# Optimization experiments

Hardware: AMD Instinct MI355X
Metric: run time of the kernel (lower is better)

## Reference

```python
import jax, jax.numpy as jnp
import numpy as np

B, C_IN, C_OUT, H, W = 4, 256, 256, 56, 56
NH, K, P = 2, 5, 2
HD = C_OUT // NH          # 128
SE_H = C_OUT // 16        # 16
SE_H2 = max(SE_H // 16, 1)  # 1
EPS = 1e-5


def setup_inputs() -> dict:
    key = jax.random.key(0)
    ks = jax.random.split(key, 16)
    n = lambda k, sh, s=1.0: jax.random.normal(k, sh, jnp.float32) * s

    def bn_params(k, c):
        k1, k2 = jax.random.split(k)
        return (1.0 + 0.1 * n(k1, (c,)), 0.1 * n(k2, (c,)),
                jnp.zeros((c,), jnp.float32), jnp.ones((c,), jnp.float32))

    agg_g1, agg_b1, agg_m1, agg_v1 = bn_params(ks[6], C_OUT)
    agg_g2, agg_b2, agg_m2, agg_v2 = bn_params(ks[7], C_OUT)
    se_g_in, se_b_in, se_m_in, se_v_in = bn_params(ks[8], SE_H)
    se_g_out, se_b_out, se_m_out, se_v_out = bn_params(ks[9], C_OUT)
    return {
        "x": n(ks[0], (B, C_IN, H, W)),
        "Wq": n(ks[1], (C_OUT, C_IN), C_IN ** -0.5),
        "Wk": n(ks[2], (C_OUT, C_IN), C_IN ** -0.5),
        "Wv": n(ks[3], (C_OUT, C_IN), C_IN ** -0.5),
        "rel_h": n(ks[4], (HD, 1, 1, K, 1)),
        "rel_w": n(ks[5], (HD, 1, 1, 1, K)),
        "agg_g1": agg_g1, "agg_b1": agg_b1, "agg_m1": agg_m1, "agg_v1": agg_v1,
        "agg_W": n(ks[10], (C_OUT, C_OUT), C_OUT ** -0.5),
        "agg_g2": agg_g2, "agg_b2": agg_b2, "agg_m2": agg_m2, "agg_v2": agg_v2,
        "se_Win": n(ks[11], (SE_H, C_OUT), C_OUT ** -0.5),
        "se_g_in": se_g_in, "se_b_in": se_b_in, "se_m_in": se_m_in, "se_v_in": se_v_in,
        "se_fc1": n(ks[12], (SE_H2, SE_H), SE_H ** -0.5),
        "se_fc2": n(ks[13], (SE_H, SE_H2)),
        "se_Wout": n(ks[14], (C_OUT, SE_H), SE_H ** -0.5),
        "se_g_out": se_g_out, "se_b_out": se_b_out, "se_m_out": se_m_out, "se_v_out": se_v_out,
    }


def _conv1x1(Wm, t):
    return jnp.einsum('oc,bchw->bohw', Wm, t)


def _bn(t, g, b, m, v):
    # eval-mode BatchNorm2d with running stats
    return (t - m[:, None, None]) * (g * jax.lax.rsqrt(v + EPS))[:, None, None] + b[:, None, None]


def _windows(t):
    # (B, O, H+2P, W+2P) -> (B, O, H, W, K, K), matching torch unfold(2,K,1).unfold(3,K,1)
    w = jnp.stack([t[:, :, i:i + H, j:j + W] for i in range(K) for j in range(K)], axis=-1)
    return w.reshape(t.shape[0], t.shape[1], H, W, K, K)


def reference(x, Wq, Wk, Wv, rel_h, rel_w,
              agg_g1, agg_b1, agg_m1, agg_v1, agg_W, agg_g2, agg_b2, agg_m2, agg_v2,
              se_Win, se_g_in, se_b_in, se_m_in, se_v_in, se_fc1, se_fc2, se_Wout,
              se_g_out, se_b_out, se_m_out, se_v_out):
    xp = jnp.pad(x, ((0, 0), (0, 0), (P, P), (P, P)))
    q = _conv1x1(Wq, x).reshape(B, NH, HD, H, W)          # (B,NH,HD,H,W)
    k_win = _windows(_conv1x1(Wk, xp))                    # (B,O,H,W,K,K)
    v_win = _windows(_conv1x1(Wv, xp))
    # relative position bias: first head gets rel_h (height taps), second gets rel_w
    k_win = jnp.concatenate([k_win[:, :HD] + rel_h[None], k_win[:, HD:] + rel_w[None]], axis=1)
    k_r = k_win.reshape(B, NH, HD, H, W, K * K)
    v_r = v_win.reshape(B, NH, HD, H, W, K * K)
    scores = jnp.einsum('bnchw,bnchwk->bnhwk', q, k_r) / jnp.sqrt(jnp.float32(HD))
    attn = jax.nn.softmax(scores, axis=-1)
    out = jnp.einsum('bnhwk,bnchwk->bnchw', attn, v_r).reshape(B, C_OUT, H, W)
    # agg: BN -> ReLU -> 1x1 conv -> BN
    y = jax.nn.relu(_bn(out, agg_g1, agg_b1, agg_m1, agg_v1))
    y = _bn(_conv1x1(agg_W, y), agg_g2, agg_b2, agg_m2, agg_v2)
    # squeeze-excitation (intended math; original view(b,c) is a channel-count bug)
    s = jax.nn.relu(_bn(_conv1x1(se_Win, y), se_g_in, se_b_in, se_m_in, se_v_in))  # (B,SE_H,H,W)
    p = s.mean(axis=(2, 3))                                                        # (B,SE_H)
    g = jax.nn.sigmoid(jax.nn.relu(p @ se_fc1.T) @ se_fc2.T)                       # (B,SE_H)
    s = s * g[:, :, None, None]
    return _bn(_conv1x1(se_Wout, s), se_g_out, se_b_out, se_m_out, se_v_out)
```

## Files before the change

### kernel.cpp

```cpp
#include <hip/hip_runtime.h>
#include <hip/hip_bf16.h>

#define HW 3136
#define HH 56
#define WW 56
#define BB 4
#define CC 256
#define HD 128

#define TH 4
#define TW 8
#define WR 8
#define WC 12
#define WPX 96
#define KS2 136

#define ASTR 72

typedef __attribute__((ext_vector_type(8))) short bf16x8;
typedef __attribute__((ext_vector_type(4))) float f32x4;

__device__ __forceinline__ unsigned short f2bf(float f) {
    unsigned int u; __builtin_memcpy(&u, &f, 4);
    unsigned int r = u + 0x7FFFu + ((u >> 16) & 1u);
    return (unsigned short)(r >> 16);
}
__device__ __forceinline__ float bflo(unsigned int u) {
    unsigned int x = u << 16; float f; __builtin_memcpy(&f, &x, 4); return f;
}
__device__ __forceinline__ float bfhi(unsigned int u) {
    unsigned int x = u & 0xFFFF0000u; float f; __builtin_memcpy(&f, &x, 4); return f;
}
__device__ __forceinline__ void unpk8(uint4 u, float* f) {
    f[0] = bflo(u.x); f[1] = bfhi(u.x); f[2] = bflo(u.y); f[3] = bfhi(u.y);
    f[4] = bflo(u.z); f[5] = bfhi(u.z); f[6] = bflo(u.w); f[7] = bfhi(u.w);
}

__global__ __launch_bounds__(256) void cvt_all(
    const float* __restrict__ x,
    const float* __restrict__ Wq, const float* __restrict__ Wk,
    const float* __restrict__ Wv, const float* __restrict__ Wa,
    const float* __restrict__ Wse,
    const float* __restrict__ rel_h, const float* __restrict__ rel_w,
    unsigned short* __restrict__ xt, unsigned short* __restrict__ wb,
    float* __restrict__ psum, float* __restrict__ relws)
{
    int t = threadIdx.x;
    if (blockIdx.z == 4) {
        int bid = blockIdx.y * 49 + blockIdx.x;
        if (bid == 0 && t < 64) psum[t] = 0.f;
        if (bid == 1 && t < 128) {
#pragma unroll
            for (int tt = 0; tt < 5; tt++) {
                relws[tt * 128 + t]       = rel_h[t * 5 + tt];
                relws[640 + tt * 128 + t] = rel_w[t * 5 + tt];
            }
        }
        for (int chunk = bid; chunk < 260; chunk += 196) {
            int wsel, off;
            if (chunk < 256) { wsel = chunk >> 6; off = (chunk & 63) * 1024 + t * 4; }
            else             { wsel = 4;          off = (chunk - 256) * 1024 + t * 4; }
            const float* s = (wsel == 0) ? Wq : (wsel == 1) ? Wk :
                             (wsel == 2) ? Wv : (wsel == 3) ? Wa : Wse;
            float4 f = *(const float4*)(s + off);
            uint2 pk;
            pk.x = (unsigned int)f2bf(f.x) | ((unsigned int)f2bf(f.y) << 16);
            pk.y = (unsigned int)f2bf(f.z) | ((unsigned int)f2bf(f.w) << 16);
            *(uint2*)(wb + (size_t)wsel * 65536 + off) = pk;
        }
        return;
    }
    int b = blockIdx.z;
    int c0 = blockIdx.y * 64;
    int p0 = blockIdx.x * 64;
    __shared__ float tile[64][65];
    int p4 = t & 15, cl = t >> 4;
    const float* xb = x + ((size_t)b * CC + c0) * HW + p0;
#pragma unroll
    for (int i = 0; i < 4; i++) {
        int c = cl + 16 * i;
        float4 f = *(const float4*)(xb + (size_t)c * HW + p4 * 4);
        tile[c][p4 * 4 + 0] = f.x; tile[c][p4 * 4 + 1] = f.y;
        tile[c][p4 * 4 + 2] = f.z; tile[c][p4 * 4 + 3] = f.w;
    }
    __syncthreads();
    int c2 = t & 31, pl = t >> 5;
    unsigned short* xo = xt + ((size_t)b * HW + p0) * CC + c0;
#pragma unroll
    for (int i = 0; i < 8; i++) {
        int p = pl + 8 * i;
        float a = tile[2 * c2][p], bb = tile[2 * c2 + 1][p];
        unsigned int pk = (unsigned int)f2bf(a) | ((unsigned int)f2bf(bb) << 16);
        *(unsigned int*)(xo + (size_t)p * CC + 2 * c2) = pk;
    }
}

__global__ __launch_bounds__(256) void qkv_mfma(
    const unsigned short* __restrict__ xt, const unsigned short* __restrict__ wqkv,
    unsigned short* __restrict__ q_ws, unsigned short* __restrict__ k_ws,
    unsigned short* __restrict__ v_ws)
{
    int wsel = blockIdx.z;
    unsigned short* outp = (wsel == 0) ? q_ws : ((wsel == 1) ? k_ws : v_ws);
    int gp0 = blockIdx.x * 128, o0 = blockIdx.y * 128;

    __shared__ unsigned short As[128 * ASTR];
    __shared__ unsigned short Bs[128 * ASTR];
    const unsigned short* xb = xt + (size_t)gp0 * CC;
    const unsigned short* wbp = wqkv + (size_t)wsel * 65536 + (size_t)o0 * CC;

    int t = threadIdx.x;
    int wave = t >> 6, lane = t & 63;
    int mo = (wave & 1) * 64, no = (wave >> 1) * 64;
    int lm = lane & 15, lq = lane >> 4;
    int sr = t >> 3, sc = t & 7;

    f32x4 acc[4][4];
#pragma unroll
    for (int i = 0; i < 4; i++)
#pragma unroll
        for (int j = 0; j < 4; j++) acc[i][j] = (f32x4){0.f, 0.f, 0.f, 0.f};

    for (int k0 = 0; k0 < 256; k0 += 64) {
#pragma unroll
        for (int i = 0; i < 4; i++) {
            int r = sr + 32 * i;
            *(uint4*)&As[r * ASTR + sc * 8] = *(const uint4*)(xb + (size_t)r * CC + k0 + sc * 8);
            *(uint4*)&Bs[r * ASTR + sc * 8] = *(const uint4*)(wbp + (size_t)r * CC + k0 + sc * 8);
        }
        __syncthreads();
#pragma unroll
        for (int ks = 0; ks < 64; ks += 32) {
            bf16x8 af[4], bfr[4];
#pragma unroll
            for (int i = 0; i < 4; i++)
                af[i] = *(bf16x8*)&As[(mo + 16 * i + lm) * ASTR + ks + lq * 8];
#pragma unroll
            for (int j = 0; j < 4; j++)
                bfr[j] = *(bf16x8*)&Bs[(no + 16 * j + lm) * ASTR + ks + lq * 8];
#pragma unroll
            for (int i = 0; i < 4; i++)
#pragma unroll
                for (int j = 0; j < 4; j++)
                    acc[i][j] = __builtin_amdgcn_mfma_f32_16x16x32_bf16(
                        af[i], bfr[j], acc[i][j], 0, 0, 0);
        }
        __syncthreads();
    }
    unsigned short* ob = outp + (size_t)gp0 * CC + o0;
    bool ev = (lm & 1) == 0;
    int elm = lm & ~1;
#pragma unroll
    for (int i = 0; i < 4; i++)
#pragma unroll
        for (int j = 0; j < 4; j++)
#pragma unroll
            for (int r = 0; r < 4; r++) {
                float v = acc[i][j][r];
                float p = __shfl_xor(v, 1, 64);
                unsigned int pk = ev
                    ? ((unsigned int)f2bf(v) | ((unsigned int)f2bf(p) << 16))
                    : ((unsigned int)f2bf(p) | ((unsigned int)f2bf(v) << 16));
                if (ev == (r < 2)) {
                    int m = mo + 16 * i + lq * 4 + r;
                    int n = no + 16 * j + elm;
                    *(unsigned int*)(ob + (size_t)m * CC + n) = pk;
                }
            }
}

__global__ __launch_bounds__(256) void agg_mfma(
    const unsigned short* __restrict__ ao, const unsigned short* __restrict__ wagg,
    const float* __restrict__ g1, const float* __restrict__ b1,
    const float* __restrict__ m1, const float* __restrict__ v1,
    const float* __restrict__ g2, const float* __restrict__ b2,
    const float* __restrict__ m2, const float* __restrict__ v2,
    float* __restrict__ y2)
{
    int gp0 = blockIdx.x * 128, o0 = blockIdx.y * 128;

    __shared__ unsigned short As[128 * ASTR];
    __shared__ unsigned short Bs[128 * ASTR];
    __shared__ float s1[256], o1[256], s2[256], o2[256];

    int t = threadIdx.x;
    {
        float sc1 = g1[t] * rsqrtf(v1[t] + 1e-5f);
        s1[t] = sc1; o1[t] = b1[t] - m1[t] * sc1;
        float sc2 = g2[t] * rsqrtf(v2[t] + 1e-5f);
        s2[t] = sc2; o2[t] = b2[t] - m2[t] * sc2;
    }

    const unsigned short* aob = ao + (size_t)gp0 * CC;
    const unsigned short* wbp = wagg + (size_t)o0 * CC;

    int wave = t >> 6, lane = t & 63;
    int mo = (wave & 1) * 64, no = (wave >> 1) * 64;
    int lm = lane & 15, lq = lane >> 4;
    int sr = t >> 3, sc = t & 7;

    f32x4 acc[4][4];
#pragma unroll
    for (int i = 0; i < 4; i++)
#pragma unroll
        for (int j = 0; j < 4; j++) acc[i][j] = (f32x4){0.f, 0.f, 0.f, 0.f};

    __syncthreads();

    for (int k0 = 0; k0 < 256; k0 += 64) {
#pragma unroll
        for (int i = 0; i < 4; i++) {
            int r = sr + 32 * i;
            int cb = k0 + sc * 8;
            uint4 u = *(const uint4*)(aob + (size_t)r * CC + cb);
            float e[8] = {bflo(u.x), bfhi(u.x), bflo(u.y), bfhi(u.y),
                          bflo(u.z), bfhi(u.z), bflo(u.w), bfhi(u.w)};
            unsigned short pk[8];
#pragma unroll
            for (int uu = 0; uu < 8; uu++) {
                float vv = fmaxf(e[uu] * s1[cb + uu] + o1[cb + uu], 0.f);
                pk[uu] = f2bf(vv);
            }
            *(uint4*)&As[r * ASTR + sc * 8] = *(uint4*)pk;
            *(uint4*)&Bs[r * ASTR + sc * 8] = *(const uint4*)(wbp + (size_t)r * CC + k0 + sc * 8);
        }
        __syncthreads();
#pragma unroll
        for (int ks = 0; ks < 64; ks += 32) {
            bf16x8 af[4], bfr[4];
#pragma unroll
            for (int i = 0; i < 4; i++)
                af[i] = *(bf16x8*)&As[(mo + 16 * i + lm) * ASTR + ks + lq * 8];
#pragma unroll
            for (int j = 0; j < 4; j++)
                bfr[j] = *(bf16x8*)&Bs[(no + 16 * j + lm) * ASTR + ks + lq * 8];
#pragma unroll
            for (int i = 0; i < 4; i++)
#pragma unroll
                for (int j = 0; j < 4; j++)
                    acc[i][j] = __builtin_amdgcn_mfma_f32_16x16x32_bf16(
                        af[i], bfr[j], acc[i][j], 0, 0, 0);
        }
        __syncthreads();
    }
    float* yb = y2 + (size_t)gp0 * CC + o0;
#pragma unroll
    for (int i = 0; i < 4; i++)
#pragma unroll
        for (int j = 0; j < 4; j++)
#pragma unroll
            for (int r = 0; r < 4; r++) {
                int m = mo + 16 * i + lq * 4 + r;
                int n = no + 16 * j + lm;
                yb[(size_t)m * CC + n] = acc[i][j][r] * s2[o0 + n] + o2[o0 + n];
            }
}

__global__ __launch_bounds__(256) void attn_kernel(
    const unsigned short* __restrict__ q_ws, const unsigned short* __restrict__ k_ws,
    const unsigned short* __restrict__ v_ws,
    const float* __restrict__ relws,
    unsigned short* __restrict__ ao_ws)
{
    __shared__ unsigned short kwin[WPX * KS2];
    __shared__ unsigned short vwin[WPX * KS2];

    int t = threadIdx.x;
    int tile = blockIdx.x;
    int n = blockIdx.y;
    int b = blockIdx.z;
    int tr = tile / 7, tc = tile - tr * 7;
    int h0 = tr * TH, w0 = tc * TW;
    const size_t base = (size_t)b * HW * CC + n * HD;
    const float* relp = relws + n * 640;

    {
        int c8 = t & 15, pw0 = t >> 4;
#pragma unroll
        for (int it = 0; it < 6; it++) {
            int pw = pw0 + it * 16;
            int wr = pw / 12, wc = pw - wr * 12;
            int gh = h0 + wr - 2, gw = w0 + wc - 2;
            uint4 uk = make_uint4(0u, 0u, 0u, 0u);
            uint4 uv = make_uint4(0u, 0u, 0u, 0u);
            if (gh >= 0 && gh < HH && gw >= 0 && gw < WW) {
                size_t off = base + (size_t)(gh * WW + gw) * CC + c8 * 8;
                uk = *(const uint4*)(k_ws + off);
                uv = *(const uint4*)(v_ws + off);
            }
            *(uint4*)&kwin[pw * KS2 + c8 * 8] = uk;
            *(uint4*)&vwin[pw * KS2 + c8 * 8] = uv;
        }
    }

    int px = t >> 3, c4g = t & 7;
    int pr = px >> 3, pc = px & 7;
    int ghp = h0 + pr, gwp = w0 + pc;
    const size_t pbase = base + (size_t)(ghp * WW + gwp) * CC;

    float qf[16];
    {
        uint4 u0 = *(const uint4*)(q_ws + pbase + c4g * 16);
        uint4 u1 = *(const uint4*)(q_ws + pbase + c4g * 16 + 8);
        unpk8(u0, qf); unpk8(u1, qf + 8);
    }

    float acc[30];
#pragma unroll
    for (int tt = 0; tt < 5; tt++) {
        float s = 0.f;
#pragma unroll
        for (int j = 0; j < 4; j++) {
            float4 r4 = *(const float4*)(relp + tt * 128 + c4g * 16 + j * 4);
            s += qf[j * 4 + 0] * r4.x + qf[j * 4 + 1] * r4.y
               + qf[j * 4 + 2] * r4.z + qf[j * 4 + 3] * r4.w;
        }
        acc[25 + tt] = s;
    }

    __syncthreads();

#pragma unroll
    for (int tt = 0; tt < 25; tt++) {
        int di = tt / 5, dj = tt - 5 * di;
        const unsigned short* kp = &kwin[((pr + di) * WC + pc + dj) * KS2 + c4g * 16];
        float kf[16];
        unpk8(*(const uint4*)kp, kf);
        unpk8(*(const uint4*)(kp + 8), kf + 8);
        float s = 0.f;
#pragma unroll
        for (int c = 0; c < 16; c++) s += qf[c] * kf[c];
        acc[tt] = s;
    }

#pragma unroll
    for (int tt = 0; tt < 30; tt++) {
#pragma unroll
        for (int m = 1; m < 8; m <<= 1)
            acc[tt] += __shfl_xor(acc[tt], m, 64);
    }

    {
        const float inv = 0.08838834764831845f;
        float mx = -1e30f;
#pragma unroll
        for (int tt = 0; tt < 25; tt++) {
            int di = tt / 5, dj = tt - 5 * (tt / 5);
            acc[tt] = (acc[tt] + ((n == 0) ? acc[25 + di] : acc[25 + dj])) * inv;
            mx = fmaxf(mx, acc[tt]);
        }
        float sum = 0.f;
#pragma unroll
        for (int tt = 0; tt < 25; tt++) { acc[tt] = __expf(acc[tt] - mx); sum += acc[tt]; }
        float rs = 1.f / sum;
#pragma unroll
        for (int tt = 0; tt < 25; tt++) acc[tt] *= rs;
    }

    float oacc[16];
#pragma unroll
    for (int c = 0; c < 16; c++) oacc[c] = 0.f;
#pragma unroll
    for (int tt = 0; tt < 25; tt++) {
        int di = tt / 5, dj = tt - 5 * di;
        const unsigned short* vp = &vwin[((pr + di) * WC + pc + dj) * KS2 + c4g * 16];
        float vf[16];
        unpk8(*(const uint4*)vp, vf);
        unpk8(*(const uint4*)(vp + 8), vf + 8);
        float a = acc[tt];
#pragma unroll
        for (int c = 0; c < 16; c++) oacc[c] += a * vf[c];
    }

    unsigned short pk[16];
#pragma unroll
    for (int c = 0; c < 16; c++) pk[c] = f2bf(oacc[c]);
    *(uint4*)(ao_ws + pbase + c4g * 16)     = *(uint4*)pk;
    *(uint4*)(ao_ws + pbase + c4g * 16 + 8) = *(uint4*)&pk[8];
}

__global__ __launch_bounds__(64) void se_in_mfma(
    const float* __restrict__ y2, const unsigned short* __restrict__ wse,
    const float* __restrict__ gin, const float* __restrict__ bin,
    const float* __restrict__ min_, const float* __restrict__ vin,
    float* __restrict__ s_ws, float* __restrict__ psum)
{
    int lane = threadIdx.x;
    int tile = blockIdx.x;
    int gp0 = tile * 16;
    int b = tile / 196;
    int lm = lane & 15, lq = lane >> 4;

    f32x4 acc = (f32x4){0.f, 0.f, 0.f, 0.f};
    const float* ya = y2 + (size_t)(gp0 + lm) * CC;
#pragma unroll
    for (int k0 = 0; k0 < 256; k0 += 32) {
        int kb = k0 + lq * 8;
        float4 f0 = *(const float4*)(ya + kb);
        float4 f1 = *(const float4*)(ya + kb + 4);
        unsigned short pk[8] = {f2bf(f0.x), f2bf(f0.y), f2bf(f0.z), f2bf(f0.w),
                                f2bf(f1.x), f2bf(f1.y), f2bf(f1.z), f2bf(f1.w)};
        bf16x8 af = *(bf16x8*)pk;
        bf16x8 bf = *(const bf16x8*)(wse + (size_t)lm * CC + kb);
        acc = __builtin_amdgcn_mfma_f32_16x16x32_bf16(af, bf, acc, 0, 0, 0);
    }
    float sc = gin[lm] * rsqrtf(vin[lm] + 1e-5f);
    float off = bin[lm] - min_[lm] * sc;
    float sum4 = 0.f;
#pragma unroll
    for (int r = 0; r < 4; r++) {
        int row = lq * 4 + r;
        float v = fmaxf(acc[r] * sc + off, 0.f);
        s_ws[(size_t)(gp0 + row) * 16 + lm] = v;
        sum4 += v;
    }
    sum4 += __shfl_xor(sum4, 16, 64);
    sum4 += __shfl_xor(sum4, 32, 64);
    if (lane < 16) atomicAdd(&psum[b * 16 + lane], sum4);
}

__global__ __launch_bounds__(256) void se_out_kernel(
    const float* __restrict__ s_ws, const float* __restrict__ psum,
    const float* __restrict__ fc1, const float* __restrict__ fc2,
    const float* __restrict__ se_Wout,
    const float* __restrict__ gout, const float* __restrict__ bout,
    const float* __restrict__ mout, const float* __restrict__ vout,
    float* __restrict__ out)
{
    int b = blockIdx.y;
    int px0 = blockIdx.x * 32;
    __shared__ float sl[32 * 17];
    __shared__ float wg[256 * 20];
    __shared__ float bo[256];
    __shared__ float gg[16];
    int t = threadIdx.x;

    if (t < 16) {
        float h = 0.f;
#pragma unroll
        for (int jj = 0; jj < 16; jj++)
            h += (psum[b * 16 + jj] * (1.f / 3136.f)) * fc1[jj];
        h = fmaxf(h, 0.f);
        float z = h * fc2[t];
        gg[t] = 1.f / (1.f + __expf(-z));
    }
    {
        const float* sb = s_ws + (size_t)(b * HW + px0) * 16;
#pragma unroll
        for (int i = 0; i < 2; i++) {
            int idx = t + 256 * i;
            sl[(idx >> 4) * 17 + (idx & 15)] = sb[idx];
        }
    }
    __syncthreads();
    {
        float sc = gout[t] * rsqrtf(vout[t] + 1e-5f);
        bo[t] = bout[t] - mout[t] * sc;
        const float* wr = se_Wout + (size_t)t * 16;
#pragma unroll
        for (int k = 0; k < 16; k++)
            wg[t * 20 + k] = wr[k] * gg[k] * sc;
    }
    __syncthreads();

    int px = t & 31, og = t >> 5;
    float4 s0 = *(float4*)&sl[px * 17 + 0];
    float4 s1v = *(float4*)&sl[px * 17 + 4];
    float4 s2v = *(float4*)&sl[px * 17 + 8];
    float4 s3 = *(float4*)&sl[px * 17 + 12];
    float* ob = out + (size_t)b * CC * HW + px0 + px;
#pragma unroll
    for (int oi = 0; oi < 32; oi++) {
        int o = og * 32 + oi;
        float4 w0 = *(float4*)&wg[o * 20 + 0];
        float4 w1 = *(float4*)&wg[o * 20 + 4];
        float4 w2 = *(float4*)&wg[o * 20 + 8];
        float4 w3 = *(float4*)&wg[o * 20 + 12];
        float r = bo[o]
            + s0.x * w0.x + s0.y * w0.y + s0.z * w0.z + s0.w * w0.w
            + s1v.x * w1.x + s1v.y * w1.y + s1v.z * w1.z + s1v.w * w1.w
            + s2v.x * w2.x + s2v.y * w2.y + s2v.z * w2.z + s2v.w * w2.w
            + s3.x * w3.x + s3.y * w3.y + s3.z * w3.z + s3.w * w3.w;
        ob[(size_t)o * HW] = r;
    }
}

extern "C" void kernel_launch(void* const* d_in, const int* in_sizes, int n_in,
                              void* d_out, int out_size, void* d_ws, size_t ws_size,
                              hipStream_t stream) {
    const float* x     = (const float*)d_in[0];
    const float* Wq    = (const float*)d_in[1];
    const float* Wk    = (const float*)d_in[2];
    const float* Wv    = (const float*)d_in[3];
    const float* rel_h = (const float*)d_in[4];
    const float* rel_w = (const float*)d_in[5];
    const float* agg_g1 = (const float*)d_in[6];
    const float* agg_b1 = (const float*)d_in[7];
    const float* agg_m1 = (const float*)d_in[8];
    const float* agg_v1 = (const float*)d_in[9];
    const float* agg_W  = (const float*)d_in[10];
    const float* agg_g2 = (const float*)d_in[11];
    const float* agg_b2 = (const float*)d_in[12];
    const float* agg_m2 = (const float*)d_in[13];
    const float* agg_v2 = (const float*)d_in[14];
    const float* se_Win = (const float*)d_in[15];
    const float* se_g_in = (const float*)d_in[16];
    const float* se_b_in = (const float*)d_in[17];
    const float* se_m_in = (const float*)d_in[18];
    const float* se_v_in = (const float*)d_in[19];
    const float* se_fc1  = (const float*)d_in[20];
    const float* se_fc2  = (const float*)d_in[21];
    const float* se_Wout = (const float*)d_in[22];
    const float* se_g_out = (const float*)d_in[23];
    const float* se_b_out = (const float*)d_in[24];
    const float* se_m_out = (const float*)d_in[25];
    const float* se_v_out = (const float*)d_in[26];

    const size_t NQ = (size_t)BB * HW * CC;
    unsigned short* q_ws  = (unsigned short*)d_ws;
    unsigned short* k_ws  = q_ws + NQ;
    unsigned short* v_ws  = k_ws + NQ;
    unsigned short* ao_ws = v_ws + NQ;
    unsigned short* xt    = ao_ws;
    float* y2_ws = (float*)d_ws;
    float* s_ws  = (float*)(ao_ws + NQ);
    float* psum  = s_ws + (size_t)BB * HW * 16;
    unsigned short* wbf = (unsigned short*)(psum + 64);
    float* relws = (float*)(wbf + 4 * 65536 + 4096);

    cvt_all<<<dim3(49, 4, 5), 256, 0, stream>>>(x, Wq, Wk, Wv, agg_W, se_Win,
                                                rel_h, rel_w, xt, wbf, psum, relws);
    qkv_mfma<<<dim3(98, 2, 3), 256, 0, stream>>>(xt, wbf, q_ws, k_ws, v_ws);
    attn_kernel<<<dim3(98, 2, 4), 256, 0, stream>>>(q_ws, k_ws, v_ws, relws, ao_ws);
    agg_mfma<<<dim3(98, 2), 256, 0, stream>>>(ao_ws, wbf + 3 * 65536,
        agg_g1, agg_b1, agg_m1, agg_v1, agg_g2, agg_b2, agg_m2, agg_v2, y2_ws);
    se_in_mfma<<<dim3(784), 64, 0, stream>>>(y2_ws, wbf + 4 * 65536,
        se_g_in, se_b_in, se_m_in, se_v_in, s_ws, psum);
    se_out_kernel<<<dim3(98, 4), 256, 0, stream>>>(s_ws, psum, se_fc1, se_fc2,
        se_Wout, se_g_out, se_b_out, se_m_out, se_v_out, (float*)d_out);
}
```

Before: 203.2 us.

## Fuse input conversion into QKV GEMM and merge agg with SE-in

Removes the separate conversion kernel. The QKV GEMM now reads fp32 x and weights directly, transposing and converting to bf16 while staging into shared memory. The agg 1x1 conv and the SE input conv are merged into one kernel that keeps the agg output in LDS as bf16, so the fp32 y2 round trip through global memory goes away. The attention kernel reads rel_h and rel_w in their original layout. In exchange, each QKV block re-converts its weights and does strided fp32 x loads, and agg_se uses smaller 32-pixel tiles that reload the full weight matrix per block.

Result: no change. 207.0 us (+1.9%).

```diff
diff --git a/kernel.cpp b/kernel.cpp
--- a/kernel.cpp
+++ b/kernel.cpp
@@ -16,6 +16,7 @@
 #define KS2 136
 
 #define ASTR 72
+#define YSTR 264
 
 typedef __attribute__((ext_vector_type(8))) short bf16x8;
 typedef __attribute__((ext_vector_type(4))) float f32x4;
@@ -35,86 +36,44 @@
     f[0] = bflo(u.x); f[1] = bfhi(u.x); f[2] = bflo(u.y); f[3] = bfhi(u.y);
     f[4] = bflo(u.z); f[5] = bfhi(u.z); f[6] = bflo(u.w); f[7] = bfhi(u.w);
 }
-
-__global__ __launch_bounds__(256) void cvt_all(
+__device__ __forceinline__ uint4 pack8(float4 a, float4 b) {
+    uint4 pk;
+    pk.x = (unsigned int)f2bf(a.x) | ((unsigned int)f2bf(a.y) << 16);
+    pk.y = (unsigned int)f2bf(a.z) | ((unsigned int)f2bf(a.w) << 16);
+    pk.z = (unsigned int)f2bf(b.x) | ((unsigned int)f2bf(b.y) << 16);
+    pk.w = (unsigned int)f2bf(b.z) | ((unsigned int)f2bf(b.w) << 16);
+    return pk;
+}
+
+__global__ __launch_bounds__(256) void qkv_direct(
     const float* __restrict__ x,
     const float* __restrict__ Wq, const float* __restrict__ Wk,
-    const float* __restrict__ Wv, const float* __restrict__ Wa,
-    const float* __restrict__ Wse,
-    const float* __restrict__ rel_h, const float* __restrict__ rel_w,
-    unsigned short* __restrict__ xt, unsigned short* __restrict__ wb,
-    float* __restrict__ psum, float* __restrict__ relws)
-{
-    int t = threadIdx.x;
-    if (blockIdx.z == 4) {
-        int bid = blockIdx.y * 49 + blockIdx.x;
-        if (bid == 0 && t < 64) psum[t] = 0.f;
-        if (bid == 1 && t < 128) {
-#pragma unroll
-            for (int tt = 0; tt < 5; tt++) {
-                relws[tt * 128 + t]       = rel_h[t * 5 + tt];
-                relws[640 + tt * 128 + t] = rel_w[t * 5 + tt];
-            }
-        }
-        for (int chunk = bid; chunk < 260; chunk += 196) {
-            int wsel, off;
-            if (chunk < 256) { wsel = chunk >> 6; off = (chunk & 63) * 1024 + t * 4; }
-            else             { wsel = 4;          off = (chunk - 256) * 1024 + t * 4; }
-            const float* s = (wsel == 0) ? Wq : (wsel == 1) ? Wk :
-                             (wsel == 2) ? Wv : (wsel == 3) ? Wa : Wse;
-            float4 f = *(const float4*)(s + off);
-            uint2 pk;
-            pk.x = (unsigned int)f2bf(f.x) | ((unsigned int)f2bf(f.y) << 16);
-            pk.y = (unsigned int)f2bf(f.z) | ((unsigned int)f2bf(f.w) << 16);
-            *(uint2*)(wb + (size_t)wsel * 65536 + off) = pk;
-        }
-        return;
-    }
-    int b = blockIdx.z;
-    int c0 = blockIdx.y * 64;
-    int p0 = blockIdx.x * 64;
-    __shared__ float tile[64][65];
-    int p4 = t & 15, cl = t >> 4;
-    const float* xb = x + ((size_t)b * CC + c0) * HW + p0;
-#pragma unroll
-    for (int i = 0; i < 4; i++) {
-        int c = cl + 16 * i;
-        float4 f = *(const float4*)(xb + (size_t)c * HW + p4 * 4);
-        tile[c][p4 * 4 + 0] = f.x; tile[c][p4 * 4 + 1] = f.y;
-        tile[c][p4 * 4 + 2] = f.z; tile[c][p4 * 4 + 3] = f.w;
-    }
-    __syncthreads();
-    int c2 = t & 31, pl = t >> 5;
-    unsigned short* xo = xt + ((size_t)b * HW + p0) * CC + c0;
-#pragma unroll
-    for (int i = 0; i < 8; i++) {
-        int p = pl + 8 * i;
-        float a = tile[2 * c2][p], bb = tile[2 * c2 + 1][p];
-        unsigned int pk = (unsigned int)f2bf(a) | ((unsigned int)f2bf(bb) << 16);
-        *(unsigned int*)(xo + (size_t)p * CC + 2 * c2) = pk;
-    }
-}
-
-__global__ __launch_bounds__(256) void qkv_mfma(
-    const unsigned short* __restrict__ xt, const unsigned short* __restrict__ wqkv,
+    const float* __restrict__ Wv,
     unsigned short* __restrict__ q_ws, unsigned short* __restrict__ k_ws,
-    unsigned short* __restrict__ v_ws)
+    unsigned short* __restrict__ v_ws, float* __restrict__ psum)
 {
     int wsel = blockIdx.z;
+    const float* wsrc = (wsel == 0) ? Wq : ((wsel == 1) ? Wk : Wv);
     unsigned short* outp = (wsel == 0) ? q_ws : ((wsel == 1) ? k_ws : v_ws);
     int gp0 = blockIdx.x * 128, o0 = blockIdx.y * 128;
+    int t = threadIdx.x;
+
+    if (blockIdx.x == 0 && blockIdx.y == 0 && wsel == 0 && t < 64) psum[t] = 0.f;
 
     __shared__ unsigned short As[128 * ASTR];
     __shared__ unsigned short Bs[128 * ASTR];
-    const unsigned short* xb = xt + (size_t)gp0 * CC;
-    const unsigned short* wbp = wqkv + (size_t)wsel * 65536 + (size_t)o0 * CC;
-
-    int t = threadIdx.x;
+
     int wave = t >> 6, lane = t & 63;
     int mo = (wave & 1) * 64, no = (wave >> 1) * 64;
     int lm = lane & 15, lq = lane >> 4;
     int sr = t >> 3, sc = t & 7;
 
+    int tpx = t & 31, tch = t >> 5;
+    int gpa = gp0 + 4 * tpx;
+    int ba = gpa / HW;
+    int pa = gpa - ba * HW;
+    const float* xb = x + (size_t)ba * CC * HW + pa;
+
     f32x4 acc[4][4];
 #pragma unroll
     for (int i = 0; i < 4; i++)
@@ -125,8 +84,25 @@
 #pragma unroll
         for (int i = 0; i < 4; i++) {
             int r = sr + 32 * i;
-            *(uint4*)&As[r * ASTR + sc * 8] = *(const uint4*)(xb + (size_t)r * CC + k0 + sc * 8);
-            *(uint4*)&Bs[r * ASTR + sc * 8] = *(const uint4*)(wbp + (size_t)r * CC + k0 + sc * 8);
+            const float* wr = wsrc + (size_t)(o0 + r) * CC + k0 + sc * 8;
+            float4 w0 = *(const float4*)wr;
+            float4 w1 = *(const float4*)(wr + 4);
+            *(uint4*)&Bs[r * ASTR + sc * 8] = pack8(w0, w1);
+        }
+#pragma unroll
+        for (int i = 0; i < 4; i++) {
+            int cr = 2 * tch + 16 * i;
+            int c = k0 + cr;
+            float4 f0 = *(const float4*)(xb + (size_t)c * HW);
+            float4 f1 = *(const float4*)(xb + (size_t)(c + 1) * HW);
+            const float* p0 = (const float*)&f0;
+            const float* p1 = (const float*)&f1;
+#pragma unroll
+            for (int j = 0; j < 4; j++) {
+                unsigned int pk = (unsigned int)f2bf(p0[j]) |
+                                  ((unsigned int)f2bf(p1[j]) << 16);
+                *(unsigned int*)&As[(4 * tpx + j) * ASTR + cr] = pk;
+            }
         }
         __syncthreads();
 #pragma unroll
@@ -169,97 +145,10 @@
             }
 }
 
-__global__ __launch_bounds__(256) void agg_mfma(
-    const unsigned short* __restrict__ ao, const unsigned short* __restrict__ wagg,
-    const float* __restrict__ g1, const float* __restrict__ b1,
-    const float* __restrict__ m1, const float* __restrict__ v1,
-    const float* __restrict__ g2, const float* __restrict__ b2,
-    const float* __restrict__ m2, const float* __restrict__ v2,
-    float* __restrict__ y2)
-{
-    int gp0 = blockIdx.x * 128, o0 = blockIdx.y * 128;
-
-    __shared__ unsigned short As[128 * ASTR];
-    __shared__ unsigned short Bs[128 * ASTR];
-    __shared__ float s1[256], o1[256], s2[256], o2[256];
-
-    int t = threadIdx.x;
-    {
-        float sc1 = g1[t] * rsqrtf(v1[t] + 1e-5f);
-        s1[t] = sc1; o1[t] = b1[t] - m1[t] * sc1;
-        float sc2 = g2[t] * rsqrtf(v2[t] + 1e-5f);
-        s2[t] = sc2; o2[t] = b2[t] - m2[t] * sc2;
-    }
-
-    const unsigned short* aob = ao + (size_t)gp0 * CC;
-    const unsigned short* wbp = wagg + (size_t)o0 * CC;
-
-    int wave = t >> 6, lane = t & 63;
-    int mo = (wave & 1) * 64, no = (wave >> 1) * 64;
-    int lm = lane & 15, lq = lane >> 4;
-    int sr = t >> 3, sc = t & 7;
-
-    f32x4 acc[4][4];
-#pragma unroll
-    for (int i = 0; i < 4; i++)
-#pragma unroll
-        for (int j = 0; j < 4; j++) acc[i][j] = (f32x4){0.f, 0.f, 0.f, 0.f};
-
-    __syncthreads();
-
-    for (int k0 = 0; k0 < 256; k0 += 64) {
-#pragma unroll
-        for (int i = 0; i < 4; i++) {
-            int r = sr + 32 * i;
-            int cb = k0 + sc * 8;
-            uint4 u = *(const uint4*)(aob + (size_t)r * CC + cb);
-            float e[8] = {bflo(u.x), bfhi(u.x), bflo(u.y), bfhi(u.y),
-                          bflo(u.z), bfhi(u.z), bflo(u.w), bfhi(u.w)};
-            unsigned short pk[8];
-#pragma unroll
-            for (int uu = 0; uu < 8; uu++) {
-                float vv = fmaxf(e[uu] * s1[cb + uu] + o1[cb + uu], 0.f);
-                pk[uu] = f2bf(vv);
-            }
-            *(uint4*)&As[r * ASTR + sc * 8] = *(uint4*)pk;
-            *(uint4*)&Bs[r * ASTR + sc * 8] = *(const uint4*)(wbp + (size_t)r * CC + k0 + sc * 8);
-        }
-        __syncthreads();
-#pragma unroll
-        for (int ks = 0; ks < 64; ks += 32) {
-            bf16x8 af[4], bfr[4];
-#pragma unroll
-            for (int i = 0; i < 4; i++)
-                af[i] = *(bf16x8*)&As[(mo + 16 * i + lm) * ASTR + ks + lq * 8];
-#pragma unroll
-            for (int j = 0; j < 4; j++)
-                bfr[j] = *(bf16x8*)&Bs[(no + 16 * j + lm) * ASTR + ks + lq * 8];
-#pragma unroll
-            for (int i = 0; i < 4; i++)
-#pragma unroll
-                for (int j = 0; j < 4; j++)
-                    acc[i][j] = __builtin_amdgcn_mfma_f32_16x16x32_bf16(
-                        af[i], bfr[j], acc[i][j], 0, 0, 0);
-        }
-        __syncthreads();
-    }
-    float* yb = y2 + (size_t)gp0 * CC + o0;
-#pragma unroll
-    for (int i = 0; i < 4; i++)
-#pragma unroll
-        for (int j = 0; j < 4; j++)
-#pragma unroll
-            for (int r = 0; r < 4; r++) {
-                int m = mo + 16 * i + lq * 4 + r;
-                int n = no + 16 * j + lm;
-                yb[(size_t)m * CC + n] = acc[i][j][r] * s2[o0 + n] + o2[o0 + n];
-            }
-}
-
 __global__ __launch_bounds__(256) void attn_kernel(
     const unsigned short* __restrict__ q_ws, const unsigned short* __restrict__ k_ws,
     const unsigned short* __restrict__ v_ws,
-    const float* __restrict__ relws,
+    const float* __restrict__ rel_h, const float* __restrict__ rel_w,
     unsigned short* __restrict__ ao_ws)
 {
     __shared__ unsigned short kwin[WPX * KS2];
@@ -272,7 +161,7 @@
     int tr = tile / 7, tc = tile - tr * 7;
     int h0 = tr * TH, w0 = tc * TW;
     const size_t base = (size_t)b * HW * CC + n * HD;
-    const float* relp = relws + n * 640;
+    const float* relp = (n == 0) ? rel_h : rel_w;
 
     {
         int c8 = t & 15, pw0 = t >> 4;
@@ -307,15 +196,17 @@
 
     float acc[30];
 #pragma unroll
-    for (int tt = 0; tt < 5; tt++) {
-        float s = 0.f;
-#pragma unroll
-        for (int j = 0; j < 4; j++) {
-            float4 r4 = *(const float4*)(relp + tt * 128 + c4g * 16 + j * 4);
-            s += qf[j * 4 + 0] * r4.x + qf[j * 4 + 1] * r4.y
-               + qf[j * 4 + 2] * r4.z + qf[j * 4 + 3] * r4.w;
-        }
-        acc[25 + tt] = s;
+    for (int tt = 0; tt < 5; tt++) acc[25 + tt] = 0.f;
+    {
+        int c0 = c4g * 16;
+#pragma unroll
+        for (int c = 0; c < 16; c++) {
+            const float* rr = relp + (size_t)(c0 + c) * 5;
+            float qc = qf[c];
+            acc[25] += qc * rr[0]; acc[26] += qc * rr[1];
+            acc[27] += qc * rr[2]; acc[28] += qc * rr[3];
+            acc[29] += qc * rr[4];
+        }
     }
 
     __syncthreads();
@@ -379,44 +270,133 @@
     *(uint4*)(ao_ws + pbase + c4g * 16 + 8) = *(uint4*)&pk[8];
 }
 
-__global__ __launch_bounds__(64) void se_in_mfma(
-    const float* __restrict__ y2, const unsigned short* __restrict__ wse,
+__global__ __launch_bounds__(256) void agg_se(
+    const unsigned short* __restrict__ ao, const float* __restrict__ Wa,
+    const float* __restrict__ g1, const float* __restrict__ b1,
+    const float* __restrict__ m1, const float* __restrict__ v1,
+    const float* __restrict__ g2, const float* __restrict__ b2,
+    const float* __restrict__ m2, const float* __restrict__ v2,
+    const float* __restrict__ Wse,
     const float* __restrict__ gin, const float* __restrict__ bin,
     const float* __restrict__ min_, const float* __restrict__ vin,
     float* __restrict__ s_ws, float* __restrict__ psum)
 {
-    int lane = threadIdx.x;
-    int tile = blockIdx.x;
-    int gp0 = tile * 16;
-    int b = tile / 196;
+    int gp0 = blockIdx.x * 32;
+    __shared__ unsigned short As[32 * ASTR];
+    __shared__ unsigned short Bs[256 * ASTR];
+    __shared__ unsigned short ybuf[32 * YSTR];
+    __shared__ float s1[256], o1[256], s2[256], o2[256];
+
+    int t = threadIdx.x;
+    {
+        float sc1 = g1[t] * rsqrtf(v1[t] + 1e-5f);
+        s1[t] = sc1; o1[t] = b1[t] - m1[t] * sc1;
+        float sc2 = g2[t] * rsqrtf(v2[t] + 1e-5f);
+        s2[t] = sc2; o2[t] = b2[t] - m2[t] * sc2;
+    }
+
+    int wave = t >> 6, lane = t & 63;
     int lm = lane & 15, lq = lane >> 4;
-
-    f32x4 acc = (f32x4){0.f, 0.f, 0.f, 0.f};
-    const float* ya = y2 + (size_t)(gp0 + lm) * CC;
-#pragma unroll
-    for (int k0 = 0; k0 < 256; k0 += 32) {
-        int kb = k0 + lq * 8;
-        float4 f0 = *(const float4*)(ya + kb);
-        float4 f1 = *(const float4*)(ya + kb + 4);
-        unsigned short pk[8] = {f2bf(f0.x), f2bf(f0.y), f2bf(f0.z), f2bf(f0.w),
-                                f2bf(f1.x), f2bf(f1.y), f2bf(f1.z), f2bf(f1.w)};
-        bf16x8 af = *(bf16x8*)pk;
-        bf16x8 bf = *(const bf16x8*)(wse + (size_t)lm * CC + kb);
-        acc = __builtin_amdgcn_mfma_f32_16x16x32_bf16(af, bf, acc, 0, 0, 0);
-    }
-    float sc = gin[lm] * rsqrtf(vin[lm] + 1e-5f);
-    float off = bin[lm] - min_[lm] * sc;
-    float sum4 = 0.f;
-#pragma unroll
-    for (int r = 0; r < 4; r++) {
-        int row = lq * 4 + r;
-        float v = fmaxf(acc[r] * sc + off, 0.f);
-        s_ws[(size_t)(gp0 + row) * 16 + lm] = v;
-        sum4 += v;
-    }
-    sum4 += __shfl_xor(sum4, 16, 64);
-    sum4 += __shfl_xor(sum4, 32, 64);
-    if (lane < 16) atomicAdd(&psum[b * 16 + lane], sum4);
+    int asr = t >> 3, asc = t & 7;
+
+    f32x4 acc[2][4];
+#pragma unroll
+    for (int i = 0; i < 2; i++)
+#pragma unroll
+        for (int j = 0; j < 4; j++) acc[i][j] = (f32x4){0.f, 0.f, 0.f, 0.f};
+
+    __syncthreads();
+
+    for (int k0 = 0; k0 < 256; k0 += 64) {
+        {
+            int cb = k0 + asc * 8;
+            uint4 u = *(const uint4*)(ao + (size_t)(gp0 + asr) * CC + cb);
+            float e[8]; unpk8(u, e);
+            unsigned short pk[8];
+#pragma unroll
+            for (int uu = 0; uu < 8; uu++)
+                pk[uu] = f2bf(fmaxf(e[uu] * s1[cb + uu] + o1[cb + uu], 0.f));
+            *(uint4*)&As[asr * ASTR + asc * 8] = *(uint4*)pk;
+        }
+#pragma unroll
+        for (int i = 0; i < 8; i++) {
+            int r = asr + 32 * i;
+            const float* wr = Wa + (size_t)r * CC + k0 + asc * 8;
+            float4 w0 = *(const float4*)wr;
+            float4 w1 = *(const float4*)(wr + 4);
+            *(uint4*)&Bs[r * ASTR + asc * 8] = pack8(w0, w1);
+        }
+        __syncthreads();
+#pragma unroll
+        for (int ks = 0; ks < 64; ks += 32) {
+            bf16x8 af[2], bfr[4];
+#pragma unroll
+            for (int i = 0; i < 2; i++)
+                af[i] = *(bf16x8*)&As[(16 * i + lm) * ASTR + ks + lq * 8];
+#pragma unroll
+            for (int j = 0; j < 4; j++)
+                bfr[j] = *(bf16x8*)&Bs[(wave * 64 + 16 * j + lm) * ASTR + ks + lq * 8];
+#pragma unroll
+            for (int i = 0; i < 2; i++)
+#pragma unroll
+                for (int j = 0; j < 4; j++)
+                    acc[i][j] = __builtin_amdgcn_mfma_f32_16x16x32_bf16(
+                        af[i], bfr[j], acc[i][j], 0, 0, 0);
+        }
+        __syncthreads();
+    }
+
+    {
+        bool ev = (lm & 1) == 0;
+        int elm = lm & ~1;
+#pragma unroll
+        for (int i = 0; i < 2; i++)
+#pragma unroll
+            for (int j = 0; j < 4; j++)
+#pragma unroll
+                for (int r = 0; r < 4; r++) {
+                    int nf = wave * 64 + 16 * j + lm;
+                    float v = acc[i][j][r] * s2[nf] + o2[nf];
+                    float p = __shfl_xor(v, 1, 64);
+                    unsigned int pk = ev
+                        ? ((unsigned int)f2bf(v) | ((unsigned int)f2bf(p) << 16))
+                        : ((unsigned int)f2bf(p) | ((unsigned int)f2bf(v) << 16));
+                    if (ev == (r < 2)) {
+                        int m = 16 * i + lq * 4 + r;
+                        int nn = wave * 64 + 16 * j + elm;
+                        *(unsigned int*)&ybuf[m * YSTR + nn] = pk;
+                    }
+                }
+    }
+    __syncthreads();
+
+    if (wave < 2) {
+        f32x4 sa = (f32x4){0.f, 0.f, 0.f, 0.f};
+#pragma unroll
+        for (int k0 = 0; k0 < 256; k0 += 32) {
+            bf16x8 a = *(bf16x8*)&ybuf[(wave * 16 + lm) * YSTR + k0 + lq * 8];
+            const float* wr = Wse + (size_t)lm * CC + k0 + lq * 8;
+            float4 w0 = *(const float4*)wr;
+            float4 w1 = *(const float4*)(wr + 4);
+            uint4 pw = pack8(w0, w1);
+            bf16x8 bw = *(bf16x8*)&pw;
+            sa = __builtin_amdgcn_mfma_f32_16x16x32_bf16(a, bw, sa, 0, 0, 0);
+        }
+        float scn = gin[lm] * rsqrtf(vin[lm] + 1e-5f);
+        float offn = bin[lm] - min_[lm] * scn;
+        int b = gp0 / HW;
+        float part = 0.f;
+#pragma unroll
+        for (int r = 0; r < 4; r++) {
+            int px = wave * 16 + lq * 4 + r;
+            float sv = fmaxf(sa[r] * scn + offn, 0.f);
+            s_ws[(size_t)(gp0 + px) * 16 + lm] = sv;
+            part += sv;
+        }
+        part += __shfl_xor(part, 16, 64);
+        part += __shfl_xor(part, 32, 64);
+        if (lane < 16) atomicAdd(&psum[b * 16 + lane], part);
+    }
 }
 
 __global__ __launch_bounds__(256) void se_out_kernel(
@@ -521,21 +501,16 @@
     unsigned short* k_ws  = q_ws + NQ;
     unsigned short* v_ws  = k_ws + NQ;
     unsigned short* ao_ws = v_ws + NQ;
-    unsigned short* xt    = ao_ws;
-    float* y2_ws = (float*)d_ws;
     float* s_ws  = (float*)(ao_ws + NQ);
     float* psum  = s_ws + (size_t)BB * HW * 16;
-    unsigned short* wbf = (unsigned short*)(psum + 64);
-    float* relws = (float*)(wbf + 4 * 65536 + 4096);
-
-    cvt_all<<<dim3(49, 4, 5), 256, 0, stream>>>(x, Wq, Wk, Wv, agg_W, se_Win,
-                                                rel_h, rel_w, xt, wbf, psum, relws);
-    qkv_mfma<<<dim3(98, 2, 3), 256, 0, stream>>>(xt, wbf, q_ws, k_ws, v_ws);
-    attn_kernel<<<dim3(98, 2, 4), 256, 0, stream>>>(q_ws, k_ws, v_ws, relws, ao_ws);
-    agg_mfma<<<dim3(98, 2), 256, 0, stream>>>(ao_ws, wbf + 3 * 65536,
-        agg_g1, agg_b1, agg_m1, agg_v1, agg_g2, agg_b2, agg_m2, agg_v2, y2_ws);
-    se_in_mfma<<<dim3(784), 64, 0, stream>>>(y2_ws, wbf + 4 * 65536,
-        se_g_in, se_b_in, se_m_in, se_v_in, s_ws, psum);
+
+    qkv_direct<<<dim3(98, 2, 3), 256, 0, stream>>>(x, Wq, Wk, Wv,
+                                                   q_ws, k_ws, v_ws, psum);
+    attn_kernel<<<dim3(98, 2, 4), 256, 0, stream>>>(q_ws, k_ws, v_ws,
+                                                    rel_h, rel_w, ao_ws);
+    agg_se<<<dim3(392), 256, 0, stream>>>(ao_ws, agg_W,
+        agg_g1, agg_b1, agg_m1, agg_v1, agg_g2, agg_b2, agg_m2, agg_v2,
+        se_Win, se_g_in, se_b_in, se_m_in, se_v_in, s_ws, psum);
     se_out_kernel<<<dim3(98, 4), 256, 0, stream>>>(s_ws, psum, se_fc1, se_fc2,
         se_Wout, se_g_out, se_b_out, se_m_out, se_v_out, (float*)d_out);
 }
```
